# Kernel optimization log

Hardware: AMD Instinct MI355X
Metric: run time of the kernel (lower is better)

## Reference

```python
import jax, jax.numpy as jnp
import numpy as np

B, S, C_IN, E, H, DFF = 16, 1024, 4, 128, 8, 512
C1 = E * 4
DH = E // H
EPS = 1e-5


def _layer_norm(x, g, b):
    m = x.mean(-1, keepdims=True)
    v = ((x - m) ** 2).mean(-1, keepdims=True)
    return (x - m) / jnp.sqrt(v + EPS) * g + b


def _forward(x, conv1_w, conv1_b, bn1_g, bn1_b, bn1_m, bn1_v,
             conv2_w, conv2_b, bn2_g, bn2_b, bn2_m, bn2_v,
             wq, wk, wv, rel_bias, ln_attn_g, ln_attn_b,
             ln1_g, ln1_b, ff_w1, ff_b1, ff_w2, ff_b2, ln2_g, ln2_b):
    b, s, _ = x.shape
    dn = ('NCHW', 'OIHW', 'NCHW')
    h = x.transpose(0, 2, 1)[:, None]                      # [B,1,4,S]
    # Conv2d(1, 512, [1,8], padding='same') -> torch pads (3,4) on width
    h = jax.lax.conv_general_dilated(h, conv1_w, (1, 1), [(0, 0), (3, 4)], dimension_numbers=dn)
    h = h + conv1_b[None, :, None, None]
    h = (h - bn1_m[None, :, None, None]) * (bn1_g / jnp.sqrt(bn1_v + EPS))[None, :, None, None] + bn1_b[None, :, None, None]
    h = jax.nn.gelu(h, approximate=False)                  # [B,512,4,S]
    # Conv2d(512, 128, [4,1], padding='valid') collapses channel axis
    h = jax.lax.conv_general_dilated(h, conv2_w, (1, 1), [(0, 0), (0, 0)], dimension_numbers=dn)
    h = h + conv2_b[None, :, None, None]
    h = (h - bn2_m[None, :, None, None]) * (bn2_g / jnp.sqrt(bn2_v + EPS))[None, :, None, None] + bn2_b[None, :, None, None]
    h = jax.nn.gelu(h, approximate=False)                  # [B,128,1,S]
    x_src = h[:, :, 0, :].transpose(0, 2, 1)               # [B,S,E]
    # tAPE fixed positional encoding (sin/cos scaled by E/S)
    pos = jnp.arange(s, dtype=x.dtype)[:, None]
    div = jnp.exp(jnp.arange(0, E, 2, dtype=x.dtype) * (-np.log(10000.0) / E))
    ang = pos * div * (E / s)
    pe = jnp.zeros((s, E), x.dtype).at[:, 0::2].set(jnp.sin(ang)).at[:, 1::2].set(jnp.cos(ang))
    xp = x_src + pe
    # eRPE attention (Attention_Rel_Scl): scale = emb_size**-0.5, bias added POST-softmax
    q = (xp @ wq.T).reshape(b, s, H, DH).transpose(0, 2, 1, 3)
    k = (xp @ wk.T).reshape(b, s, H, DH).transpose(0, 2, 1, 3)
    v = (xp @ wv.T).reshape(b, s, H, DH).transpose(0, 2, 1, 3)
    attn = jax.nn.softmax(jnp.einsum('bhid,bhjd->bhij', q, k) * (E ** -0.5), axis=-1)
    idx = jnp.arange(s)[:, None] - jnp.arange(s)[None, :] + (s - 1)   # [S,S] in [0, 2S-2]
    attn = attn + rel_bias[idx].transpose(2, 0, 1)[None]   # [1,H,S,S]
    o = jnp.einsum('bhij,bhjd->bhid', attn, v).transpose(0, 2, 1, 3).reshape(b, s, E)
    o = _layer_norm(o, ln_attn_g, ln_attn_b)               # to_out = LayerNorm
    att = _layer_norm(x_src + o, ln1_g, ln1_b)
    ff = jax.nn.relu(att @ ff_w1.T + ff_b1) @ ff_w2.T + ff_b2
    out = _layer_norm(att + ff, ln2_g, ln2_b)
    return out.mean(axis=1)                                # GAP + flatten -> [B,E]


def setup_inputs():
    key = jax.random.key(0)
    ks = jax.random.split(key, 16)
    f32 = jnp.float32
    return {
        'x': jax.random.normal(ks[0], (B, S, C_IN), f32),
        'conv1_w': jax.random.normal(ks[1], (C1, 1, 1, 8), f32) * 0.1,
        'conv1_b': jnp.zeros((C1,), f32),
        'bn1_g': jnp.ones((C1,), f32), 'bn1_b': jnp.zeros((C1,), f32),
        'bn1_m': jax.random.normal(ks[2], (C1,), f32) * 0.01,
        'bn1_v': jax.random.uniform(ks[3], (C1,), f32, 0.5, 1.5),
        'conv2_w': jax.random.normal(ks[4], (E, C1, C_IN, 1), f32) * 0.02,
        'conv2_b': jnp.zeros((E,), f32),
        'bn2_g': jnp.ones((E,), f32), 'bn2_b': jnp.zeros((E,), f32),
        'bn2_m': jax.random.normal(ks[5], (E,), f32) * 0.01,
        'bn2_v': jax.random.uniform(ks[6], (E,), f32, 0.5, 1.5),
        'wq': jax.random.normal(ks[7], (E, E), f32) * (E ** -0.5),
        'wk': jax.random.normal(ks[8], (E, E), f32) * (E ** -0.5),
        'wv': jax.random.normal(ks[9], (E, E), f32) * (E ** -0.5),
        'rel_bias': jax.random.normal(ks[10], (2 * S - 1, H), f32) * 0.02,
        'ln_attn_g': jnp.ones((E,), f32), 'ln_attn_b': jnp.zeros((E,), f32),
        'ln1_g': jnp.ones((E,), f32), 'ln1_b': jnp.zeros((E,), f32),
        'ff_w1': jax.random.normal(ks[11], (DFF, E), f32) * (E ** -0.5),
        'ff_b1': jnp.zeros((DFF,), f32),
        'ff_w2': jax.random.normal(ks[12], (E, DFF), f32) * (DFF ** -0.5),
        'ff_b2': jnp.zeros((E,), f32),
        'ln2_g': jnp.ones((E,), f32), 'ln2_b': jnp.zeros((E,), f32),
    }


def reference(x, conv1_w, conv1_b, bn1_g, bn1_b, bn1_m, bn1_v,
              conv2_w, conv2_b, bn2_g, bn2_b, bn2_m, bn2_v,
              wq, wk, wv, rel_bias, ln_attn_g, ln_attn_b,
              ln1_g, ln1_b, ff_w1, ff_b1, ff_w2, ff_b2, ln2_g, ln2_b):
    return _forward(x, conv1_w, conv1_b, bn1_g, bn1_b, bn1_m, bn1_v,
                    conv2_w, conv2_b, bn2_g, bn2_b, bn2_m, bn2_v,
                    wq, wk, wv, rel_bias, ln_attn_g, ln_attn_b,
                    ln1_g, ln1_b, ff_w1, ff_b1, ff_w2, ff_b2, ln2_g, ln2_b)
```

## Files before the change

### kernel.cpp

```cpp
#include <hip/hip_runtime.h>
#include <hip/hip_bf16.h>
#include <math.h>

using bf16 = __hip_bfloat16;
typedef unsigned short u16;
typedef unsigned int u32;
typedef const float* __restrict__ cfp;

typedef __attribute__((ext_vector_type(8))) short short8v;
typedef __attribute__((ext_vector_type(4))) float f32x4;
typedef __attribute__((ext_vector_type(16))) float f32x16;

static constexpr int kS = 1024, kE = 128, kH = 8, kDH = 16, kDFF = 512;
static constexpr float kEps = 1e-5f;

__device__ __forceinline__ float geluf(float x) { return 0.5f * x * (1.f + erff(x * 0.70710678118654752f)); }
__device__ __forceinline__ float gelu_fast(float x) {
  float x2 = x * x;
  float u2 = 1.5957691216057308f * x * fmaf(0.044715f, x2, 1.f);
  float t = __expf(u2);
  return fmaf(-x, __frcp_rn(t + 1.f), x);
}
__device__ __forceinline__ u16 f2b(float f) {
  u32 u = __float_as_uint(f);
  u32 r = (u + 0x7FFFu + ((u >> 16) & 1u)) >> 16;
  return (u16)r;
}

template<int N> __device__ __forceinline__ void wait_vmcnt() {
  asm volatile("s_waitcnt vmcnt(%0)" :: "n"(N) : "memory");
  __builtin_amdgcn_sched_barrier(0);
}

__global__ __launch_bounds__(256) void prep_kernel(
    cfp w2, u16* __restrict__ w2b, cfp relb, u16* __restrict__ T,
    cfp fw2, u16* __restrict__ w2fb, float* __restrict__ dout) {
  int bid = blockIdx.x;
  if (bid < 128) {
    int n = bid, ck = threadIdx.x;
    const float* src = w2 + (size_t)n * 2048 + (size_t)ck * 8;
    float4 a = *(const float4*)src;
    float4 b = *(const float4*)(src + 4);
    short8v sv;
    sv[0] = (short)f2b(a.x); sv[1] = (short)f2b(a.y);
    sv[2] = (short)f2b(a.z); sv[3] = (short)f2b(a.w);
    sv[4] = (short)f2b(b.x); sv[5] = (short)f2b(b.y);
    sv[6] = (short)f2b(b.z); sv[7] = (short)f2b(b.w);
    int cd = (ck & ~7) | ((ck & 7) ^ (n & 7));
    *(short8v*)(w2b + (size_t)n * 2048 + cd * 8) = sv;
  } else if (bid < 380) {
    int idx = (bid - 128) * 4 + (threadIdx.x >> 6);
    int l = threadIdx.x & 63;
    int h = idx / 126, t = idx - h * 126;
    int lr = l & 15, lg = l >> 4;
    short8v v;
#pragma unroll
    for (int e = 0; e < 8; ++e) {
      int ix = 16 * t + 31 + lr - 8 * lg - e;
      v[e] = (short)f2b(relb[ix * 8 + h]);
    }
    *(short8v*)(T + ((size_t)(h * 126 + t) * 64 + l) * 8) = v;
  } else if (bid < 412) {
    int n = (bid - 380) * 4 + (threadIdx.x >> 6);
    int ck = threadIdx.x & 63;
    const float* src = fw2 + (size_t)n * 512 + (size_t)ck * 8;
    float4 a = *(const float4*)src;
    float4 b = *(const float4*)(src + 4);
    short8v sv;
    sv[0] = (short)f2b(a.x); sv[1] = (short)f2b(a.y);
    sv[2] = (short)f2b(a.z); sv[3] = (short)f2b(a.w);
    sv[4] = (short)f2b(b.x); sv[5] = (short)f2b(b.y);
    sv[6] = (short)f2b(b.z); sv[7] = (short)f2b(b.w);
    int cd = (ck & ~7) | ((ck & 7) ^ (n & 7));
    *(short8v*)(w2fb + (size_t)n * 512 + cd * 8) = sv;
  } else {
#pragma unroll
    for (int e = 0; e < 8; ++e) dout[threadIdx.x * 8 + e] = 0.f;
  }
}

__global__ __launch_bounds__(256) void convstage_kernel(
    cfp x, cfp w1, cfp c1b, cfp g1, cfp b1, cfp m1, cfp v1,
    u16* __restrict__ Abuf) {
  __shared__ float xs[15][4];
  int row0 = blockIdx.x * 8;
  int b = row0 >> 10, s0 = row0 & 1023;
  int tid = threadIdx.x;
  if (tid < 15) {
    int gs = s0 - 3 + tid;
    float4 xv = (gs >= 0 && gs < kS) ? ((const float4*)x)[b * kS + gs]
                                     : make_float4(0.f, 0.f, 0.f, 0.f);
    xs[tid][0] = xv.x; xs[tid][1] = xv.y; xs[tid][2] = xv.z; xs[tid][3] = xv.w;
  }
  __syncthreads();

  float w[2][8], sc[2], ofs[2], cb[2];
#pragma unroll
  for (int cc = 0; cc < 2; ++cc) {
    int cx = tid * 2 + cc;
#pragma unroll
    for (int t = 0; t < 8; ++t) w[cc][t] = w1[cx * 8 + t];
    sc[cc] = g1[cx] * __frsqrt_rn(v1[cx] + kEps);
    ofs[cc] = b1[cx] - m1[cx] * sc[cc];
    cb[cc] = c1b[cx];
  }

  for (int rl = 0; rl < 8; ++rl) {
    float ev[8];
#pragma unroll
    for (int cc = 0; cc < 2; ++cc) {
#pragma unroll
      for (int rr = 0; rr < 4; ++rr) {
        float h = cb[cc];
#pragma unroll
        for (int t = 0; t < 8; ++t) h += xs[rl + t][rr] * w[cc][t];
        ev[cc * 4 + rr] = gelu_fast(h * sc[cc] + ofs[cc]);
      }
    }
    uint4 pk;
    asm("v_cvt_pk_bf16_f32 %0, %1, %2" : "=v"(pk.x) : "v"(ev[0]), "v"(ev[1]));
    asm("v_cvt_pk_bf16_f32 %0, %1, %2" : "=v"(pk.y) : "v"(ev[2]), "v"(ev[3]));
    asm("v_cvt_pk_bf16_f32 %0, %1, %2" : "=v"(pk.z) : "v"(ev[4]), "v"(ev[5]));
    asm("v_cvt_pk_bf16_f32 %0, %1, %2" : "=v"(pk.w) : "v"(ev[6]), "v"(ev[7]));
    int ck = (tid & ~7) | ((tid & 7) ^ (rl & 7));
    *(uint4*)(Abuf + (size_t)(row0 + rl) * 2048 + ck * 8) = pk;
  }
}

__global__ __launch_bounds__(256, 2) void convgemm_kernel(
    const u16* __restrict__ Abuf, const u16* __restrict__ w2b,
    cfp c2b, cfp g2, cfp b2, cfp m2, cfp v2,
    float* __restrict__ xsrc, u16* __restrict__ xpeb) {
  __shared__ short8v lds[3840];
  const int tid = threadIdx.x;
  const int mtile = blockIdx.x;
  const int wid = tid >> 6, lane = tid & 63;
  const int lrow = lane & 15, lk = lane >> 4;
  const int m0w = (wid & 1) * 16, n0w = (wid >> 1) * 64;

  float scn[4], cc[4], dv[4];
#pragma unroll
  for (int ni = 0; ni < 4; ++ni) {
    int n = n0w + ni * 16 + lrow;
    scn[ni] = g2[n] * __frsqrt_rn(v2[n] + kEps);
    cc[ni] = (c2b[n] - m2[n]) * scn[ni] + b2[n];
    dv[ni] = __expf((float)(n >> 1) * (-0.14391156824963732f)) * 0.125f;
  }

  f32x4 acc[4];
#pragma unroll
  for (int ni = 0; ni < 4; ++ni) acc[ni] = (f32x4){0.f, 0.f, 0.f, 0.f};

  const int q = wid * 64 + lane;
  const u16* aG = Abuf + (size_t)(mtile * 32 + (q >> 3)) * 2048 + (q & 7) * 8;

  auto stage = [&](int t) {
    int buf = t % 3;
    short8v* A = lds + buf * 1280;
    __builtin_amdgcn_global_load_lds(
        (const __attribute__((address_space(1))) void*)(aG + t * 64),
        (__attribute__((address_space(3))) void*)(A + wid * 64), 16, 0, 0);
#pragma unroll
    for (int r = 0; r < 4; ++r) {
      int qq = r * 256 + q;
      const u16* g = w2b + (size_t)(qq >> 3) * 2048 + t * 64 + (qq & 7) * 8;
      __builtin_amdgcn_global_load_lds(
          (const __attribute__((address_space(1))) void*)g,
          (__attribute__((address_space(3))) void*)(A + 256 + r * 256 + wid * 64), 16, 0, 0);
    }
  };

  auto compute = [&](int t) {
    int buf = t % 3;
    const short8v* A = lds + buf * 1280;
    const short8v* B = A + 256;
#pragma unroll
    for (int ks = 0; ks < 2; ++ks) {
      int ar = m0w + lrow;
      u32 ao = ((u32)(ar * 128 + ks * 64 + lk * 16)) ^ ((u32)((ar & 7) << 4));
      short8v af = A[ao >> 4];
#pragma unroll
      for (int ni = 0; ni < 4; ++ni) {
        int br = n0w + ni * 16 + lrow;
        u32 bo = ((u32)(br * 128 + ks * 64 + lk * 16)) ^ ((u32)((br & 7) << 4));
        short8v bf = B[bo >> 4];
        acc[ni] = __builtin_amdgcn_mfma_f32_16x16x32_bf16(af, bf, acc[ni], 0, 0, 0);
      }
    }
  };

  stage(0); stage(1); stage(2);
  for (int t = 0; t < 30; ++t) {
    wait_vmcnt<10>();
    __builtin_amdgcn_s_barrier();
    __builtin_amdgcn_sched_barrier(0);
    compute(t);
    asm volatile("" ::: "memory");
    __builtin_amdgcn_s_barrier();
    __builtin_amdgcn_sched_barrier(0);
    if (t <= 28) stage(t + 3);
  }
  wait_vmcnt<5>();
  __builtin_amdgcn_s_barrier();
  __builtin_amdgcn_sched_barrier(0);
  compute(30);
  asm volatile("" ::: "memory");
  __builtin_amdgcn_s_barrier();
  __builtin_amdgcn_sched_barrier(0);
  wait_vmcnt<0>();
  __builtin_amdgcn_s_barrier();
  __builtin_amdgcn_sched_barrier(0);
  compute(31);

#pragma unroll
  for (int ni = 0; ni < 4; ++ni) {
    int n = n0w + ni * 16 + lrow;
#pragma unroll
    for (int r = 0; r < 4; ++r) {
      int grow = mtile * 32 + m0w + lk * 4 + r;
      float gv = geluf(acc[ni][r] * scn[ni] + cc[ni]);
      xsrc[(size_t)grow * kE + n] = gv;
      int s = grow & 1023;
      float ang = (float)s * dv[ni];
      float pe = (n & 1) ? __cosf(ang) : __sinf(ang);
      xpeb[(size_t)grow * kE + n] = f2b(gv + pe);
    }
  }
}

template<int ASRC, int MODE, int KTOT, int BM>
__global__ __launch_bounds__(256, 4) void gemm_kernel(
    const void* __restrict__ Ap, cfp Wf,
    cfp p0, cfp p1, cfp p2,
    void* __restrict__ Out, cfp res, int mbase) {
  constexpr int MI = BM / 32;
  __shared__ short8v Ab[BM * 8];
  __shared__ short8v Bb[512];

  int tid = threadIdx.x;
  int mtile = blockIdx.x, ntile = blockIdx.y;

  cfp Wsel = Wf;
  if (MODE == 1) Wsel = (blockIdx.z == 0) ? Wf : ((blockIdx.z == 1) ? p1 : p2);

  int wid = tid >> 6, lane = tid & 63;
  int m0w = (wid >> 1) * (BM / 2), n0w = (wid & 1) * 32;
  int lrow = lane & 15, lk = lane >> 4;

  f32x4 acc[MI][2];
#pragma unroll
  for (int mi = 0; mi < MI; ++mi)
#pragma unroll
    for (int ni = 0; ni < 2; ++ni) acc[mi][ni] = (f32x4){0.f, 0.f, 0.f, 0.f};

  for (int k0 = 0; k0 < KTOT; k0 += 64) {
    __syncthreads();
#pragma unroll
    for (int c = 0; c < BM / 32; ++c) {
      int chunk = tid + 256 * c;
      int row = chunk >> 3, kc = chunk & 7;
      int arow = mtile * BM + row;
      u32 off = ((u32)(row * 128 + kc * 16)) ^ ((u32)((row & 7) << 4));
      const u16* As = (const u16*)Ap + (size_t)arow * KTOT + k0 + kc * 8;
      Ab[off >> 4] = *(const short8v*)As;
    }
#pragma unroll
    for (int c = 0; c < 2; ++c) {
      int chunk = tid + 256 * c;
      int row = chunk >> 3, kc = chunk & 7;
      const float* Wp = Wsel + (size_t)(ntile * 64 + row) * KTOT + k0 + kc * 8;
      float4 xa = *(const float4*)Wp;
      float4 xb = *(const float4*)(Wp + 4);
      short8v sv;
      sv[0] = (short)f2b(xa.x); sv[1] = (short)f2b(xa.y);
      sv[2] = (short)f2b(xa.z); sv[3] = (short)f2b(xa.w);
      sv[4] = (short)f2b(xb.x); sv[5] = (short)f2b(xb.y);
      sv[6] = (short)f2b(xb.z); sv[7] = (short)f2b(xb.w);
      u32 off = ((u32)(row * 128 + kc * 16)) ^ ((u32)((row & 7) << 4));
      Bb[off >> 4] = sv;
    }
    __syncthreads();
#pragma unroll
    for (int ks = 0; ks < 2; ++ks) {
      short8v af[MI], bfr[2];
#pragma unroll
      for (int mi = 0; mi < MI; ++mi) {
        int row = m0w + mi * 16 + lrow;
        u32 off = ((u32)(row * 128 + ks * 64 + lk * 16)) ^ ((u32)((row & 7) << 4));
        af[mi] = Ab[off >> 4];
      }
#pragma unroll
      for (int ni = 0; ni < 2; ++ni) {
        int row = n0w + ni * 16 + lrow;
        u32 off = ((u32)(row * 128 + ks * 64 + lk * 16)) ^ ((u32)((row & 7) << 4));
        bfr[ni] = Bb[off >> 4];
      }
#pragma unroll
      for (int mi = 0; mi < MI; ++mi)
#pragma unroll
        for (int ni = 0; ni < 2; ++ni)
          acc[mi][ni] = __builtin_amdgcn_mfma_f32_16x16x32_bf16(af[mi], bfr[ni], acc[mi][ni], 0, 0, 0);
    }
  }

  const float qsc = 0.088388347648318447f * 1.4426950408889634f;
#pragma unroll
  for (int ni = 0; ni < 2; ++ni) {
    int n = ntile * 64 + n0w + ni * 16 + lrow;
    float c0 = 0.f;
    if (MODE == 2) c0 = p0[n];
#pragma unroll
    for (int mi = 0; mi < MI; ++mi) {
#pragma unroll
      for (int r = 0; r < 4; ++r) {
        int grow = mbase + mtile * BM + m0w + mi * 16 + lk * 4 + r;
        float val = acc[mi][ni][r];
        if (MODE == 1) {
          if (blockIdx.z == 0) val *= qsc;
          int s = grow & 1023, b_ = grow >> 10;
          u16* ob = (u16*)Out + (size_t)blockIdx.z * 2097152;
          ob[(((size_t)(b_ * kH + (n >> 4))) * kS + s) * kDH + (n & 15)] = f2b(val);
        } else if (MODE == 2) {
          int np = (n & ~56) | ((((n >> 3) ^ grow) & 7) << 3);
          ((u16*)Out)[(size_t)grow * kDFF + np] = f2b(fmaxf(val + c0, 0.f));
        }
      }
    }
  }
}

__global__ __launch_bounds__(256, 2) void ff2ln_kernel(
    const u16* __restrict__ Abuf, const u16* __restrict__ w2fb,
    cfp fb2, cfp l2g, cfp l2b, cfp res, float* __restrict__ dout) {
  __shared__ short8v lds[3840];
  __shared__ float st1[2][32], st2[2][32];
  __shared__ float red[128];
  const int tid = threadIdx.x;
  const int mtile = blockIdx.x;
  const int wid = tid >> 6, lane = tid & 63;
  const int lrow = lane & 15, lk = lane >> 4;
  const int m0w = (wid & 1) * 16, n0w = (wid >> 1) * 64;
  if (tid < 128) red[tid] = 0.f;

  float c0[4], gg[4], bb[4];
#pragma unroll
  for (int ni = 0; ni < 4; ++ni) {
    int n = n0w + ni * 16 + lrow;
    c0[ni] = fb2[n]; gg[ni] = l2g[n]; bb[ni] = l2b[n];
  }

  f32x4 acc[4];
#pragma unroll
  for (int ni = 0; ni < 4; ++ni) acc[ni] = (f32x4){0.f, 0.f, 0.f, 0.f};

  const int q = wid * 64 + lane;
  const u16* aG = Abuf + (size_t)(mtile * 32 + (q >> 3)) * 512 + (q & 7) * 8;

  auto stage = [&](int t) {
    int buf = t % 3;
    short8v* A = lds + buf * 1280;
    __builtin_amdgcn_global_load_lds(
        (const __attribute__((address_space(1))) void*)(aG + t * 64),
        (__attribute__((address_space(3))) void*)(A + wid * 64), 16, 0, 0);
#pragma unroll
    for (int r = 0; r < 4; ++r) {
      int qq = r * 256 + q;
      const u16* g = w2fb + (size_t)(qq >> 3) * 512 + t * 64 + (qq & 7) * 8;
      __builtin_amdgcn_global_load_lds(
          (const __attribute__((address_space(1))) void*)g,
          (__attribute__((address_space(3))) void*)(A + 256 + r * 256 + wid * 64), 16, 0, 0);
    }
  };

  auto compute = [&](int t) {
    int buf = t % 3;
    const short8v* A = lds + buf * 1280;
    const short8v* B = A + 256;
#pragma unroll
    for (int ks = 0; ks < 2; ++ks) {
      int ar = m0w + lrow;
      u32 ao = ((u32)(ar * 128 + ks * 64 + lk * 16)) ^ ((u32)((ar & 7) << 4));
      short8v af = A[ao >> 4];
#pragma unroll
      for (int ni = 0; ni < 4; ++ni) {
        int br = n0w + ni * 16 + lrow;
        u32 bo = ((u32)(br * 128 + ks * 64 + lk * 16)) ^ ((u32)((br & 7) << 4));
        short8v bf = B[bo >> 4];
        acc[ni] = __builtin_amdgcn_mfma_f32_16x16x32_bf16(af, bf, acc[ni], 0, 0, 0);
      }
    }
  };

  stage(0); stage(1); stage(2);
  for (int t = 0; t < 6; ++t) {
    wait_vmcnt<10>();
    __builtin_amdgcn_s_barrier();
    __builtin_amdgcn_sched_barrier(0);
    compute(t);
    asm volatile("" ::: "memory");
    __builtin_amdgcn_s_barrier();
    __builtin_amdgcn_sched_barrier(0);
    if (t <= 4) stage(t + 3);
  }
  wait_vmcnt<5>();
  __builtin_amdgcn_s_barrier();
  __builtin_amdgcn_sched_barrier(0);
  compute(6);
  asm volatile("" ::: "memory");
  __builtin_amdgcn_s_barrier();
  __builtin_amdgcn_sched_barrier(0);
  wait_vmcnt<0>();
  __builtin_amdgcn_s_barrier();
  __builtin_amdgcn_sched_barrier(0);
  compute(7);

  float y[4][4];
  float s1[4] = {0.f, 0.f, 0.f, 0.f}, s2[4] = {0.f, 0.f, 0.f, 0.f};
#pragma unroll
  for (int ni = 0; ni < 4; ++ni) {
    int n = n0w + ni * 16 + lrow;
#pragma unroll
    for (int r = 0; r < 4; ++r) {
      int grow = mtile * 32 + m0w + lk * 4 + r;
      float v = acc[ni][r] + c0[ni] + res[(size_t)grow * kE + n];
      y[ni][r] = v;
      s1[r] += v;
      s2[r] += v * v;
    }
  }
#pragma unroll
  for (int r = 0; r < 4; ++r) {
    for (int off = 1; off < 16; off <<= 1) {
      s1[r] += __shfl_xor(s1[r], off);
      s2[r] += __shfl_xor(s2[r], off);
    }
  }
  __syncthreads();
  if (lrow == 0) {
#pragma unroll
    for (int r = 0; r < 4; ++r) {
      int ridx = m0w + lk * 4 + r;
      st1[wid >> 1][ridx] = s1[r];
      st2[wid >> 1][ridx] = s2[r];
    }
  }
  __syncthreads();
  float colsum[4] = {0.f, 0.f, 0.f, 0.f};
#pragma unroll
  for (int r = 0; r < 4; ++r) {
    int ridx = m0w + lk * 4 + r;
    float t1 = st1[0][ridx] + st1[1][ridx];
    float t2 = st2[0][ridx] + st2[1][ridx];
    float mean = t1 * (1.f / 128.f);
    float var = t2 * (1.f / 128.f) - mean * mean;
    float inv = __frsqrt_rn(var + kEps);
#pragma unroll
    for (int ni = 0; ni < 4; ++ni)
      colsum[ni] += (y[ni][r] - mean) * inv * gg[ni] + bb[ni];
  }
#pragma unroll
  for (int ni = 0; ni < 4; ++ni) {
    colsum[ni] += __shfl_xor(colsum[ni], 16);
    colsum[ni] += __shfl_xor(colsum[ni], 32);
  }
  if (lk == 0) {
#pragma unroll
    for (int ni = 0; ni < 4; ++ni)
      atomicAdd(&red[n0w + ni * 16 + lrow], colsum[ni]);
  }
  __syncthreads();
  int b = mtile >> 5;
  if (tid < 128) atomicAdd(&dout[b * kE + tid], red[tid] * (1.f / 1024.f));
}

__global__ __launch_bounds__(512, 4) void attn_kernel(
    const u16* __restrict__ qb, const u16* __restrict__ kb,
    const u16* __restrict__ vb, const u16* __restrict__ rbT,
    float* __restrict__ o) {
  __shared__ u16 Vsh[16 * 1032];
  __shared__ u16 Pt[8][1280];

  int tid = threadIdx.x;
  int bid = blockIdx.x;
  int quarter = bid >> 7;
  int bb = (bid >> 3) & 15;
  int h = bid & 7;
  size_t base = (size_t)(bb * kH + h) * (kS * kDH);

  for (int j = tid; j < 1024; j += 512) {
    const uint4* src = (const uint4*)(vb + base + j * 16);
    uint4 a = src[0], b = src[1];
    u32 wv[8] = {a.x, a.y, a.z, a.w, b.x, b.y, b.z, b.w};
#pragma unroll
    for (int p = 0; p < 8; ++p) {
      Vsh[(2 * p) * 1032 + j]     = (u16)(wv[p] & 0xFFFFu);
      Vsh[(2 * p + 1) * 1032 + j] = (u16)(wv[p] >> 16);
    }
  }
  __syncthreads();

  int w = tid >> 6, l = tid & 63;
  int lr = l & 15, lg = l >> 4;
  int q32 = l & 31, hi = l >> 5;
  u16* P = Pt[w];
  int q0w = quarter * 256 + w * 32;
  int tbase = (q0w + 992) >> 4;
  const u16* rbh = rbT + (size_t)h * 126 * 512;

  short8v qf = *(const short8v*)(qb + base + (size_t)(q0w + q32) * 16 + hi * 8);
  short8v ones;
#pragma unroll
  for (int e = 0; e < 8; ++e) ones[e] = (short)0x3F80;

  f32x4 acc_e[2], acc_rb[2], acc_l[2];
#pragma unroll
  for (int qt = 0; qt < 2; ++qt) {
    acc_e[qt] = (f32x4){0.f, 0.f, 0.f, 0.f};
    acc_rb[qt] = (f32x4){0.f, 0.f, 0.f, 0.f};
    acc_l[qt] = (f32x4){0.f, 0.f, 0.f, 0.f};
  }
  const f32x16 z16 = {0.f,0.f,0.f,0.f,0.f,0.f,0.f,0.f,0.f,0.f,0.f,0.f,0.f,0.f,0.f,0.f};

  for (int jb = 0; jb < 32; ++jb) {
    short8v kf = *(const short8v*)(kb + base + (size_t)(jb * 32 + q32) * 16 + hi * 8);
    f32x16 s = __builtin_amdgcn_mfma_f32_32x32x16_bf16(kf, qf, z16, 0, 0, 0);
    float ev[16];
#pragma unroll
    for (int r = 0; r < 16; ++r) ev[r] = exp2f(s[r]);
#pragma unroll
    for (int rq = 0; rq < 4; ++rq) {
      u32 p0, p1;
      asm("v_cvt_pk_bf16_f32 %0, %1, %2" : "=v"(p0) : "v"(ev[4 * rq]), "v"(ev[4 * rq + 1]));
      asm("v_cvt_pk_bf16_f32 %0, %1, %2" : "=v"(p1) : "v"(ev[4 * rq + 2]), "v"(ev[4 * rq + 3]));
      *(uint2*)(P + q32 * 40 + rq * 8 + hi * 4) = make_uint2(p0, p1);
    }
    short8v vf = *(const short8v*)(Vsh + lr * 1032 + jb * 32 + lg * 8);
#pragma unroll
    for (int qt = 0; qt < 2; ++qt) {
      short8v pf = *(const short8v*)(P + (qt * 16 + lr) * 40 + lg * 8);
      int t = tbase + qt - 2 * jb;
      short8v rf = *(const short8v*)(rbh + ((size_t)t * 64 + l) * 8);
      acc_e[qt]  = __builtin_amdgcn_mfma_f32_16x16x32_bf16(pf, vf, acc_e[qt], 0, 0, 0);
      acc_l[qt]  = __builtin_amdgcn_mfma_f32_16x16x32_bf16(pf, ones, acc_l[qt], 0, 0, 0);
      acc_rb[qt] = __builtin_amdgcn_mfma_f32_16x16x32_bf16(rf, vf, acc_rb[qt], 0, 0, 0);
    }
  }

#pragma unroll
  for (int qt = 0; qt < 2; ++qt) {
#pragma unroll
    for (int r = 0; r < 4; ++r) {
      int qloc = qt * 16 + lg * 4 + r;
      int row = q0w + qloc;
      o[(size_t)(bb * kS + row) * kE + h * kDH + lr] =
          acc_e[qt][r] / acc_l[qt][r] + acc_rb[qt][r];
    }
  }
}

__global__ __launch_bounds__(256) void ln_kernel(
    cfp o, cfp xsrc, cfp lag, cfp lab, cfp l1g, cfp l1b,
    float* __restrict__ att, u16* __restrict__ attb) {
  int row = blockIdx.x * 4 + (threadIdx.x >> 6);
  int lane = threadIdx.x & 63;
  float2 a = ((const float2*)(o + (size_t)row * kE))[lane];
  float sum = a.x + a.y;
  for (int off = 1; off < 64; off <<= 1) sum += __shfl_xor(sum, off);
  float mean = sum * (1.f / 128.f);
  float d0 = a.x - mean, d1 = a.y - mean;
  float ss = d0 * d0 + d1 * d1;
  for (int off = 1; off < 64; off <<= 1) ss += __shfl_xor(ss, off);
  float inv = 1.f / sqrtf(ss * (1.f / 128.f) + kEps);
  float t0 = d0 * inv * lag[2 * lane] + lab[2 * lane];
  float t1 = d1 * inv * lag[2 * lane + 1] + lab[2 * lane + 1];
  float2 xv = ((const float2*)(xsrc + (size_t)row * kE))[lane];
  t0 += xv.x; t1 += xv.y;
  float sum2 = t0 + t1;
  for (int off = 1; off < 64; off <<= 1) sum2 += __shfl_xor(sum2, off);
  float mean2 = sum2 * (1.f / 128.f);
  float e0 = t0 - mean2, e1 = t1 - mean2;
  float ss2 = e0 * e0 + e1 * e1;
  for (int off = 1; off < 64; off <<= 1) ss2 += __shfl_xor(ss2, off);
  float inv2 = 1.f / sqrtf(ss2 * (1.f / 128.f) + kEps);
  float r0 = e0 * inv2 * l1g[2 * lane] + l1b[2 * lane];
  float r1 = e1 * inv2 * l1g[2 * lane + 1] + l1b[2 * lane + 1];
  ((float2*)(att + (size_t)row * kE))[lane] = make_float2(r0, r1);
  ((u32*)attb)[(size_t)row * 64 + lane] = (u32)f2b(r0) | ((u32)f2b(r1) << 16);
}

extern "C" void kernel_launch(void* const* d_in, const int* in_sizes, int n_in,
                              void* d_out, int out_size, void* d_ws, size_t ws_size,
                              hipStream_t stream) {
  const float* wf[27];
  for (int i = 0; i < n_in && i < 27; ++i) wf[i] = (const float*)d_in[i];

  float* ws = (float*)d_ws;
  float* xsrc  = ws;
  float* att   = xsrc + 2097152;
  float* qkv0  = att + 2097152;
  float* ext   = qkv0 + 3145728;
  float* o     = ext + 1048576;
  u16* xpeb    = (u16*)(o + 2097152);
  u16* w2b     = xpeb + 2097152;
  u16* rbT     = w2b + 262144;
  u16* w2fb    = rbT + 516096;
  u16* Abuf    = w2fb + 65536;

  u16* qb = (u16*)qkv0;
  u16* kb = qb + 2097152;
  u16* vb = kb + 2097152;
  u16* ff1b = (u16*)qkv0;
  u16* attb = xpeb;
  float* doutf = (float*)d_out;

  prep_kernel<<<413, 256, 0, stream>>>(wf[7], w2b, wf[16], rbT, wf[23], w2fb, doutf);

  convstage_kernel<<<2048, 256, 0, stream>>>(
      wf[0], wf[1], wf[2], wf[3], wf[4], wf[5], wf[6], Abuf);
  convgemm_kernel<<<512, 256, 0, stream>>>(
      Abuf, w2b, wf[8], wf[9], wf[10], wf[11], wf[12], xsrc, xpeb);

  gemm_kernel<3, 1, 128, 64><<<dim3(256, 2, 3), 256, 0, stream>>>(
      xpeb, wf[13], nullptr, wf[14], wf[15], qb, nullptr, 0);

  attn_kernel<<<512, 512, 0, stream>>>(qb, kb, vb, rbT, o);
  ln_kernel<<<4096, 256, 0, stream>>>(o, xsrc, wf[17], wf[18], wf[19], wf[20], att, attb);

  gemm_kernel<3, 2, 128, 64><<<dim3(256, 8), 256, 0, stream>>>(
      attb, wf[21], wf[22], nullptr, nullptr, ff1b, nullptr, 0);

  ff2ln_kernel<<<512, 256, 0, stream>>>(ff1b, w2fb, wf[24], wf[25], wf[26], att, doutf);
}
```

Baseline: 131.0 us.

## Pre-convert QKV/FF1 weights to bf16 and double-buffer attention P tiles

The prep kernel now converts wq/wk/wv and ff_w1 to bf16 once, so the generic GEMM loads bf16 weights directly instead of converting fp32 weights in every tile. The attention loop is software-pipelined: QK^T and exp for block jb+1 are computed while the PV MFMAs for block jb consume a double-buffered P tile in LDS. This doubles P shared memory and lowers the launch-bounds occupancy hint from 4 to 2 blocks, which may reduce latency hiding.

```diff
diff --git a/kernel.cpp b/kernel.cpp
--- a/kernel.cpp
+++ b/kernel.cpp
@@ -6,6 +6,7 @@
 typedef unsigned short u16;
 typedef unsigned int u32;
 typedef const float* __restrict__ cfp;
+typedef const u16* __restrict__ cbu;
 
 typedef __attribute__((ext_vector_type(8))) short short8v;
 typedef __attribute__((ext_vector_type(4))) float f32x4;
@@ -34,7 +35,9 @@
 
 __global__ __launch_bounds__(256) void prep_kernel(
     cfp w2, u16* __restrict__ w2b, cfp relb, u16* __restrict__ T,
-    cfp fw2, u16* __restrict__ w2fb, float* __restrict__ dout) {
+    cfp fw2, u16* __restrict__ w2fb, float* __restrict__ dout,
+    cfp wq, cfp wk, cfp wv, u16* __restrict__ wqkvb,
+    cfp fw1, u16* __restrict__ w1fb) {
   int bid = blockIdx.x;
   if (bid < 128) {
     int n = bid, ck = threadIdx.x;
@@ -73,9 +76,32 @@
     sv[6] = (short)f2b(b.z); sv[7] = (short)f2b(b.w);
     int cd = (ck & ~7) | ((ck & 7) ^ (n & 7));
     *(short8v*)(w2fb + (size_t)n * 512 + cd * 8) = sv;
+  } else if (bid < 413) {
+#pragma unroll
+    for (int e = 0; e < 8; ++e) dout[threadIdx.x * 8 + e] = 0.f;
+  } else if (bid < 437) {
+    int g = (bid - 413) * 256 + threadIdx.x;
+    int z = g >> 11, local = g & 2047;
+    const float* src = ((z == 0) ? wq : (z == 1) ? wk : wv) + (size_t)local * 8;
+    float4 a = *(const float4*)src;
+    float4 b = *(const float4*)(src + 4);
+    short8v sv;
+    sv[0] = (short)f2b(a.x); sv[1] = (short)f2b(a.y);
+    sv[2] = (short)f2b(a.z); sv[3] = (short)f2b(a.w);
+    sv[4] = (short)f2b(b.x); sv[5] = (short)f2b(b.y);
+    sv[6] = (short)f2b(b.z); sv[7] = (short)f2b(b.w);
+    *(short8v*)(wqkvb + (size_t)z * 16384 + local * 8) = sv;
   } else {
-#pragma unroll
-    for (int e = 0; e < 8; ++e) dout[threadIdx.x * 8 + e] = 0.f;
+    int g = (bid - 437) * 256 + threadIdx.x;
+    const float* src = fw1 + (size_t)g * 8;
+    float4 a = *(const float4*)src;
+    float4 b = *(const float4*)(src + 4);
+    short8v sv;
+    sv[0] = (short)f2b(a.x); sv[1] = (short)f2b(a.y);
+    sv[2] = (short)f2b(a.z); sv[3] = (short)f2b(a.w);
+    sv[4] = (short)f2b(b.x); sv[5] = (short)f2b(b.y);
+    sv[6] = (short)f2b(b.z); sv[7] = (short)f2b(b.w);
+    *(short8v*)(w1fb + (size_t)g * 8) = sv;
   }
 }
 
@@ -230,8 +256,8 @@
 
 template<int ASRC, int MODE, int KTOT, int BM>
 __global__ __launch_bounds__(256, 4) void gemm_kernel(
-    const void* __restrict__ Ap, cfp Wf,
-    cfp p0, cfp p1, cfp p2,
+    const void* __restrict__ Ap, cbu Wf,
+    cfp p0, cbu p1, cbu p2,
     void* __restrict__ Out, cfp res, int mbase) {
   constexpr int MI = BM / 32;
   __shared__ short8v Ab[BM * 8];
@@ -240,7 +266,7 @@
   int tid = threadIdx.x;
   int mtile = blockIdx.x, ntile = blockIdx.y;
 
-  cfp Wsel = Wf;
+  cbu Wsel = Wf;
   if (MODE == 1) Wsel = (blockIdx.z == 0) ? Wf : ((blockIdx.z == 1) ? p1 : p2);
 
   int wid = tid >> 6, lane = tid & 63;
@@ -268,16 +294,9 @@
     for (int c = 0; c < 2; ++c) {
       int chunk = tid + 256 * c;
       int row = chunk >> 3, kc = chunk & 7;
-      const float* Wp = Wsel + (size_t)(ntile * 64 + row) * KTOT + k0 + kc * 8;
-      float4 xa = *(const float4*)Wp;
-      float4 xb = *(const float4*)(Wp + 4);
-      short8v sv;
-      sv[0] = (short)f2b(xa.x); sv[1] = (short)f2b(xa.y);
-      sv[2] = (short)f2b(xa.z); sv[3] = (short)f2b(xa.w);
-      sv[4] = (short)f2b(xb.x); sv[5] = (short)f2b(xb.y);
-      sv[6] = (short)f2b(xb.z); sv[7] = (short)f2b(xb.w);
+      const u16* Wp = Wsel + (size_t)(ntile * 64 + row) * KTOT + k0 + kc * 8;
       u32 off = ((u32)(row * 128 + kc * 16)) ^ ((u32)((row & 7) << 4));
-      Bb[off >> 4] = sv;
+      Bb[off >> 4] = *(const short8v*)Wp;
     }
     __syncthreads();
 #pragma unroll
@@ -473,12 +492,12 @@
   if (tid < 128) atomicAdd(&dout[b * kE + tid], red[tid] * (1.f / 1024.f));
 }
 
-__global__ __launch_bounds__(512, 4) void attn_kernel(
+__global__ __launch_bounds__(512, 2) void attn_kernel(
     const u16* __restrict__ qb, const u16* __restrict__ kb,
     const u16* __restrict__ vb, const u16* __restrict__ rbT,
     float* __restrict__ o) {
   __shared__ u16 Vsh[16 * 1032];
-  __shared__ u16 Pt[8][1280];
+  __shared__ u16 Pt[8][2560];
 
   int tid = threadIdx.x;
   int bid = blockIdx.x;
@@ -521,9 +540,7 @@
   }
   const f32x16 z16 = {0.f,0.f,0.f,0.f,0.f,0.f,0.f,0.f,0.f,0.f,0.f,0.f,0.f,0.f,0.f,0.f};
 
-  for (int jb = 0; jb < 32; ++jb) {
-    short8v kf = *(const short8v*)(kb + base + (size_t)(jb * 32 + q32) * 16 + hi * 8);
-    f32x16 s = __builtin_amdgcn_mfma_f32_32x32x16_bf16(kf, qf, z16, 0, 0, 0);
+  auto expand_store = [&](const f32x16& s, int bufoff) {
     float ev[16];
 #pragma unroll
     for (int r = 0; r < 16; ++r) ev[r] = exp2f(s[r]);
@@ -532,18 +549,34 @@
       u32 p0, p1;
       asm("v_cvt_pk_bf16_f32 %0, %1, %2" : "=v"(p0) : "v"(ev[4 * rq]), "v"(ev[4 * rq + 1]));
       asm("v_cvt_pk_bf16_f32 %0, %1, %2" : "=v"(p1) : "v"(ev[4 * rq + 2]), "v"(ev[4 * rq + 3]));
-      *(uint2*)(P + q32 * 40 + rq * 8 + hi * 4) = make_uint2(p0, p1);
+      *(uint2*)(P + bufoff + q32 * 40 + rq * 8 + hi * 4) = make_uint2(p0, p1);
+    }
+  };
+
+  {
+    short8v kf = *(const short8v*)(kb + base + (size_t)(0 * 32 + q32) * 16 + hi * 8);
+    f32x16 s = __builtin_amdgcn_mfma_f32_32x32x16_bf16(kf, qf, z16, 0, 0, 0);
+    expand_store(s, 0);
+  }
+
+  for (int jb = 0; jb < 32; ++jb) {
+    int cur = (jb & 1) * 1280;
+    f32x16 s2;
+    if (jb < 31) {
+      short8v kf2 = *(const short8v*)(kb + base + (size_t)((jb + 1) * 32 + q32) * 16 + hi * 8);
+      s2 = __builtin_amdgcn_mfma_f32_32x32x16_bf16(kf2, qf, z16, 0, 0, 0);
     }
     short8v vf = *(const short8v*)(Vsh + lr * 1032 + jb * 32 + lg * 8);
 #pragma unroll
     for (int qt = 0; qt < 2; ++qt) {
-      short8v pf = *(const short8v*)(P + (qt * 16 + lr) * 40 + lg * 8);
+      short8v pf = *(const short8v*)(P + cur + (qt * 16 + lr) * 40 + lg * 8);
       int t = tbase + qt - 2 * jb;
       short8v rf = *(const short8v*)(rbh + ((size_t)t * 64 + l) * 8);
       acc_e[qt]  = __builtin_amdgcn_mfma_f32_16x16x32_bf16(pf, vf, acc_e[qt], 0, 0, 0);
       acc_l[qt]  = __builtin_amdgcn_mfma_f32_16x16x32_bf16(pf, ones, acc_l[qt], 0, 0, 0);
       acc_rb[qt] = __builtin_amdgcn_mfma_f32_16x16x32_bf16(rf, vf, acc_rb[qt], 0, 0, 0);
     }
+    if (jb < 31) expand_store(s2, 1280 - cur);
   }
 
 #pragma unroll
@@ -605,6 +638,8 @@
   u16* rbT     = w2b + 262144;
   u16* w2fb    = rbT + 516096;
   u16* Abuf    = w2fb + 65536;
+  u16* wqkvb   = Abuf + 33554432;
+  u16* w1fb    = wqkvb + 49152;
 
   u16* qb = (u16*)qkv0;
   u16* kb = qb + 2097152;
@@ -613,7 +648,8 @@
   u16* attb = xpeb;
   float* doutf = (float*)d_out;
 
-  prep_kernel<<<413, 256, 0, stream>>>(wf[7], w2b, wf[16], rbT, wf[23], w2fb, doutf);
+  prep_kernel<<<469, 256, 0, stream>>>(wf[7], w2b, wf[16], rbT, wf[23], w2fb, doutf,
+                                       wf[13], wf[14], wf[15], wqkvb, wf[21], w1fb);
 
   convstage_kernel<<<2048, 256, 0, stream>>>(
       wf[0], wf[1], wf[2], wf[3], wf[4], wf[5], wf[6], Abuf);
@@ -621,13 +657,13 @@
       Abuf, w2b, wf[8], wf[9], wf[10], wf[11], wf[12], xsrc, xpeb);
 
   gemm_kernel<3, 1, 128, 64><<<dim3(256, 2, 3), 256, 0, stream>>>(
-      xpeb, wf[13], nullptr, wf[14], wf[15], qb, nullptr, 0);
+      xpeb, wqkvb, nullptr, wqkvb + 16384, wqkvb + 32768, qb, nullptr, 0);
 
   attn_kernel<<<512, 512, 0, stream>>>(qb, kb, vb, rbT, o);
   ln_kernel<<<4096, 256, 0, stream>>>(o, xsrc, wf[17], wf[18], wf[19], wf[20], att, attb);
 
   gemm_kernel<3, 2, 128, 64><<<dim3(256, 8), 256, 0, stream>>>(
-      attb, wf[21], wf[22], nullptr, nullptr, ff1b, nullptr, 0);
+      attb, w1fb, wf[22], nullptr, nullptr, ff1b, nullptr, 0);
 
   ff2ln_kernel<<<512, 256, 0, stream>>>(ff1b, w2fb, wf[24], wf[25], wf[26], att, doutf);
 }
```

Measured after the change: 130.8 us. Within noise of the previous version (-0.2%).
